# Optimization experiments

Measured on AMD Instinct MI355X. Metric: run time of the kernel, lower is better.

Reference implementation:

```python
import jax, jax.numpy as jnp
import numpy as np

PAD_IDX = 1  # matches init_kwargs pad_idx
TLEN, BATCH, D_IN = 50, 16, 512
SRC_LEN, VOCAB, CVOCAB = 200, 20000, 20400


def setup_inputs() -> dict:
    key = jax.random.key(0)
    k1, k2, k3, k4, k5, k6, k7 = jax.random.split(key, 7)
    hidden = jax.random.normal(k1, (TLEN, BATCH, D_IN), dtype=jnp.float32)
    attn = jax.random.uniform(k2, (TLEN, BATCH, SRC_LEN), dtype=jnp.float32)
    # src_map is a sparse one-hot indicator: each source position maps to one extended-vocab id
    src_ids = jax.random.randint(k3, (SRC_LEN, BATCH), 0, CVOCAB)
    src_map = jax.nn.one_hot(src_ids, CVOCAB, dtype=jnp.float32)  # (src_len, batch, cvocab)
    s = 1.0 / np.sqrt(D_IN)
    W = jax.random.uniform(k4, (VOCAB, D_IN), dtype=jnp.float32, minval=-s, maxval=s)
    b = jax.random.uniform(k5, (VOCAB,), dtype=jnp.float32, minval=-s, maxval=s)
    Wc = jax.random.uniform(k6, (1, D_IN), dtype=jnp.float32, minval=-s, maxval=s)
    bc = jax.random.uniform(k7, (1,), dtype=jnp.float32, minval=-s, maxval=s)
    return {"hidden": hidden, "attn": attn, "src_map": src_map, "W": W, "b": b, "Wc": Wc, "bc": bc}


def reference(hidden, attn, src_map, W, b, Wc, bc):
    tlen, batch, _ = hidden.shape
    src_len, _, cvocab = src_map.shape
    logits = jnp.einsum('tbd,vd->tbv', hidden, W) + b            # (tlen, batch, vocab)
    # faithful to torch: logits[:, pad_idx] = -inf (indexes the batch dim!)
    logits = logits.at[:, PAD_IDX, :].set(-jnp.inf)
    prob = jax.nn.softmax(logits, axis=1)                        # softmax over dim 1, as in source
    p_copy = jax.nn.sigmoid(jnp.einsum('tbd,od->tbo', hidden, Wc) + bc)  # (tlen, batch, 1)
    out_prob = prob * (1.0 - p_copy)                             # (tlen, batch, vocab)
    mul_attn = attn * p_copy                                     # (tlen, batch, src_len)
    # bmm over batch with one-hot src_map: effectively a scatter-add into extended vocab
    copy_prob = jnp.einsum('tbs,sbv->tbv', mul_attn, src_map)    # (tlen, batch, cvocab)
    # faithful to the split/stack/transpose permutation in the source
    flat = copy_prob.reshape(tlen * batch, cvocab)
    copy_prob = flat.reshape(batch, tlen, cvocab).swapaxes(0, 1) # (tlen, batch, cvocab)
    copy_prob = copy_prob.at[:, :, :out_prob.shape[2]].add(out_prob)
    return copy_prob
```

## Files before the change

kernel.cpp:

```cpp
#include <hip/hip_runtime.h>
#include <cstdint>
#include <cstddef>

#define TLEN    50
#define BATCH   16
#define D_IN    512
#define SRC_LEN 200
#define VOCAB   20000
#define CVOCAB  20400

typedef __bf16 bf16x8 __attribute__((ext_vector_type(8)));
typedef float  f32x4  __attribute__((ext_vector_type(4)));

#define GEMM_BLOCKS 625
#define ZERO_BLOCKS 40
#define SCAN_BLOCKS (SRC_LEN * BATCH)
#define NT 128

__global__ __launch_bounds__(256)
void pc_kernel(const float* __restrict__ hidden,
               const float* __restrict__ Wc,
               const float* __restrict__ bc,
               float* __restrict__ pc,
               __bf16* __restrict__ hbf)
{
    const int row  = blockIdx.x * 4 + (threadIdx.x >> 6);
    const int lane = threadIdx.x & 63;
    const float* h = hidden + (size_t)row * D_IN + lane * 8;
    float4 h0 = *(const float4*)(h);
    float4 h1 = *(const float4*)(h + 4);
    bf16x8 hb;
    hb[0] = (__bf16)h0.x; hb[1] = (__bf16)h0.y;
    hb[2] = (__bf16)h0.z; hb[3] = (__bf16)h0.w;
    hb[4] = (__bf16)h1.x; hb[5] = (__bf16)h1.y;
    hb[6] = (__bf16)h1.z; hb[7] = (__bf16)h1.w;
    *(bf16x8*)(hbf + (size_t)row * D_IN + lane * 8) = hb;

    float4 w0 = *(const float4*)(Wc + lane * 8);
    float4 w1 = *(const float4*)(Wc + lane * 8 + 4);
    float s = h0.x*w0.x + h0.y*w0.y + h0.z*w0.z + h0.w*w0.w
            + h1.x*w1.x + h1.y*w1.y + h1.z*w1.z + h1.w*w1.w;
    #pragma unroll
    for (int o = 1; o < 64; o <<= 1) s += __shfl_xor(s, o);
    if (lane == 0) pc[row] = 1.0f / (1.0f + __expf(-(s + bc[0])));
}

__global__ __launch_bounds__(NT)
void fused_main(const __bf16* __restrict__ hbf,
                const float* __restrict__ src_map,
                const float* __restrict__ W,
                const float* __restrict__ pc,
                float* __restrict__ out,
                int* __restrict__ src_ids)
{
    const int bid = blockIdx.x;
    const int tid = threadIdx.x;

    if (bid < GEMM_BLOCKS) {
        const int lane = tid & 63;
        const int wv   = tid >> 6;
        const int l15  = lane & 15;
        const int q    = lane >> 4;
        const int colbase = bid * 32 + wv * 16;

        bf16x8 bfrag[16];
        {
            const float* wrow = W + (size_t)(colbase + l15) * D_IN + q * 8;
            #pragma unroll
            for (int c = 0; c < 16; ++c) {
                float4 f0 = *(const float4*)(wrow + c * 32);
                float4 f1 = *(const float4*)(wrow + c * 32 + 4);
                bf16x8 bf;
                bf[0] = (__bf16)f0.x; bf[1] = (__bf16)f0.y;
                bf[2] = (__bf16)f0.z; bf[3] = (__bf16)f0.w;
                bf[4] = (__bf16)f1.x; bf[5] = (__bf16)f1.y;
                bf[6] = (__bf16)f1.z; bf[7] = (__bf16)f1.w;
                bfrag[c] = bf;
            }
            #pragma unroll
            for (int c = 0; c < 16; ++c) {
                f32x4 t = *(f32x4*)&bfrag[c];
                asm volatile("" : "+v"(t));
                bfrag[c] = *(bf16x8*)&t;
            }
        }

        for (int t = 0; t < TLEN; ++t) {
            const __bf16* arow = hbf + ((size_t)t * BATCH + l15) * D_IN + q * 8;
            f32x4 accA = {0.f, 0.f, 0.f, 0.f};
            f32x4 accB = {0.f, 0.f, 0.f, 0.f};
            #pragma unroll
            for (int c = 0; c < 16; c += 2) {
                bf16x8 a0 = *(const bf16x8*)(arow + c * 32);
                bf16x8 a1 = *(const bf16x8*)(arow + c * 32 + 32);
                accA = __builtin_amdgcn_mfma_f32_16x16x32_bf16(a0, bfrag[c],     accA, 0, 0, 0);
                accB = __builtin_amdgcn_mfma_f32_16x16x32_bf16(a1, bfrag[c + 1], accB, 0, 0, 0);
            }
            f32x4 acc = accA + accB;

            float4 pc4 = *(const float4*)(pc + t * 16 + q * 4);

            float mx = -INFINITY;
            #pragma unroll
            for (int r = 0; r < 4; ++r)
                if (q * 4 + r != 1) mx = fmaxf(mx, acc[r]);
            mx = fmaxf(mx, __shfl_xor(mx, 16));
            mx = fmaxf(mx, __shfl_xor(mx, 32));
            float e[4], s = 0.f;
            #pragma unroll
            for (int r = 0; r < 4; ++r) {
                e[r] = (q * 4 + r == 1) ? 0.f : __expf(acc[r] - mx);
                s += e[r];
            }
            s += __shfl_xor(s, 16);
            s += __shfl_xor(s, 32);
            const float inv = 1.0f / s;
            const int v = colbase + l15;
            #pragma unroll
            for (int r = 0; r < 4; ++r) {
                const int b = q * 4 + r;
                out[(size_t)(t * BATCH + b) * CVOCAB + v] = e[r] * inv * (1.0f - pc4[r]);
            }
        }
    } else if (bid < GEMM_BLOCKS + ZERO_BLOCKS) {
        const int zb = bid - GEMM_BLOCKS;
        const float4 z = {0.f, 0.f, 0.f, 0.f};
        for (int i = tid; i < 2000; i += NT) {
            const int f = zb * 2000 + i;
            const int r = f / 100;
            const int c = f % 100;
            *(float4*)(out + (size_t)r * CVOCAB + VOCAB + c * 4) = z;
        }
    } else {
        const int row = bid - GEMM_BLOCKS - ZERO_BLOCKS;
        const float4* base = (const float4*)(src_map + (size_t)row * CVOCAB);
        int found = -1;
        for (int i0 = tid; i0 < 1275; i0 += NT) {
            float4 x0 = base[i0];
            float4 x1 = base[i0 + 1275];
            float4 x2 = base[i0 + 2550];
            float4 x3 = base[i0 + 3825];
            #pragma unroll
            for (int seg = 0; seg < 4; ++seg) {
                float4 x = seg == 0 ? x0 : seg == 1 ? x1 : seg == 2 ? x2 : x3;
                const int e0 = (i0 + seg * 1275) * 4;
                if (x.x > 0.5f) found = e0;
                if (x.y > 0.5f) found = e0 + 1;
                if (x.z > 0.5f) found = e0 + 2;
                if (x.w > 0.5f) found = e0 + 3;
            }
        }
        if (found >= 0) src_ids[row] = found;
    }
}

__global__ __launch_bounds__(256)
void scatter_copy(const float* __restrict__ attn,
                  const float* __restrict__ pc,
                  const int* __restrict__ src_ids,
                  float* __restrict__ out)
{
    const int p  = blockIdx.x;
    const int si = threadIdx.x;
    if (si >= SRC_LEN) return;
    const int b  = p & 15;
    const size_t obase = (size_t)((p % TLEN) * BATCH + (p / TLEN)) * CVOCAB;
    const int id = src_ids[si * BATCH + b];
    const float val = attn[(size_t)p * SRC_LEN + si] * pc[p];
    if ((unsigned)id < (unsigned)CVOCAB)
        atomicAdd(out + obase + id, val);
}

extern "C" void kernel_launch(void* const* d_in, const int* in_sizes, int n_in,
                              void* d_out, int out_size, void* d_ws, size_t ws_size,
                              hipStream_t stream)
{
    const float* hidden  = (const float*)d_in[0];
    const float* attn    = (const float*)d_in[1];
    const float* src_map = (const float*)d_in[2];
    const float* W       = (const float*)d_in[3];
    const float* Wc      = (const float*)d_in[5];
    const float* bc      = (const float*)d_in[6];
    float* out   = (float*)d_out;

    int*    src_ids = (int*)d_ws;
    float*  pc      = (float*)((char*)d_ws + 12800);
    __bf16* hbf     = (__bf16*)((char*)d_ws + 16000);

    pc_kernel<<<dim3(200), dim3(256), 0, stream>>>(hidden, Wc, bc, pc, hbf);
    fused_main<<<dim3(GEMM_BLOCKS + ZERO_BLOCKS + SCAN_BLOCKS), dim3(NT), 0, stream>>>(
        hbf, src_map, W, pc, out, src_ids);
    scatter_copy<<<dim3(TLEN * BATCH), dim3(256), 0, stream>>>(attn, pc, src_ids, out);
}
```

Baseline: 524.0 us.

## Stage W tile in LDS and split timesteps across four waves per block

```diff
diff --git a/kernel.cpp b/kernel.cpp
--- a/kernel.cpp
+++ b/kernel.cpp
@@ -15,7 +15,7 @@
 #define GEMM_BLOCKS 625
 #define ZERO_BLOCKS 40
 #define SCAN_BLOCKS (SRC_LEN * BATCH)
-#define NT 128
+#define NT 256
 
 __global__ __launch_bounds__(256)
 void pc_kernel(const float* __restrict__ hidden,
@@ -57,69 +57,77 @@
     const int tid = threadIdx.x;
 
     if (bid < GEMM_BLOCKS) {
+        __shared__ __align__(16) __bf16 Blds[2 * 16 * 64 * 8];
+
         const int lane = tid & 63;
         const int wv   = tid >> 6;
         const int l15  = lane & 15;
         const int q    = lane >> 4;
-        const int colbase = bid * 32 + wv * 16;
-
-        bf16x8 bfrag[16];
+        const int colbase = bid * 32;
+
         {
-            const float* wrow = W + (size_t)(colbase + l15) * D_IN + q * 8;
-            #pragma unroll
-            for (int c = 0; c < 16; ++c) {
-                float4 f0 = *(const float4*)(wrow + c * 32);
-                float4 f1 = *(const float4*)(wrow + c * 32 + 4);
+            #pragma unroll
+            for (int j = 0; j < 8; ++j) {
+                const int p = wv * 8 + j;
+                const int g = p >> 4;
+                const int c = p & 15;
+                const float* src = W + (size_t)(colbase + g * 16 + l15) * D_IN
+                                     + q * 8 + c * 32;
+                float4 f0 = *(const float4*)(src);
+                float4 f1 = *(const float4*)(src + 4);
                 bf16x8 bf;
                 bf[0] = (__bf16)f0.x; bf[1] = (__bf16)f0.y;
                 bf[2] = (__bf16)f0.z; bf[3] = (__bf16)f0.w;
                 bf[4] = (__bf16)f1.x; bf[5] = (__bf16)f1.y;
                 bf[6] = (__bf16)f1.z; bf[7] = (__bf16)f1.w;
-                bfrag[c] = bf;
-            }
+                *(bf16x8*)(Blds + (size_t)(g * 16 + c) * 512 + lane * 8) = bf;
+            }
+        }
+        __syncthreads();
+
+        const int tb0 = wv * 12 + (wv < 2 ? wv : 2);
+        const int tb1 = tb0 + (wv < 2 ? 13 : 12);
+
+        for (int t = tb0; t < tb1; ++t) {
+            const __bf16* arow = hbf + ((size_t)t * BATCH + l15) * D_IN + q * 8;
+            f32x4 acc0 = {0.f, 0.f, 0.f, 0.f};
+            f32x4 acc1 = {0.f, 0.f, 0.f, 0.f};
             #pragma unroll
             for (int c = 0; c < 16; ++c) {
-                f32x4 t = *(f32x4*)&bfrag[c];
-                asm volatile("" : "+v"(t));
-                bfrag[c] = *(bf16x8*)&t;
-            }
-        }
-
-        for (int t = 0; t < TLEN; ++t) {
-            const __bf16* arow = hbf + ((size_t)t * BATCH + l15) * D_IN + q * 8;
-            f32x4 accA = {0.f, 0.f, 0.f, 0.f};
-            f32x4 accB = {0.f, 0.f, 0.f, 0.f};
-            #pragma unroll
-            for (int c = 0; c < 16; c += 2) {
-                bf16x8 a0 = *(const bf16x8*)(arow + c * 32);
-                bf16x8 a1 = *(const bf16x8*)(arow + c * 32 + 32);
-                accA = __builtin_amdgcn_mfma_f32_16x16x32_bf16(a0, bfrag[c],     accA, 0, 0, 0);
-                accB = __builtin_amdgcn_mfma_f32_16x16x32_bf16(a1, bfrag[c + 1], accB, 0, 0, 0);
-            }
-            f32x4 acc = accA + accB;
+                bf16x8 af = *(const bf16x8*)(arow + c * 32);
+                bf16x8 b0 = *(const bf16x8*)(Blds + (size_t)c * 512 + lane * 8);
+                bf16x8 b1 = *(const bf16x8*)(Blds + (size_t)(16 + c) * 512 + lane * 8);
+                acc0 = __builtin_amdgcn_mfma_f32_16x16x32_bf16(af, b0, acc0, 0, 0, 0);
+                acc1 = __builtin_amdgcn_mfma_f32_16x16x32_bf16(af, b1, acc1, 0, 0, 0);
+            }
 
             float4 pc4 = *(const float4*)(pc + t * 16 + q * 4);
 
-            float mx = -INFINITY;
-            #pragma unroll
-            for (int r = 0; r < 4; ++r)
-                if (q * 4 + r != 1) mx = fmaxf(mx, acc[r]);
-            mx = fmaxf(mx, __shfl_xor(mx, 16));
-            mx = fmaxf(mx, __shfl_xor(mx, 32));
-            float e[4], s = 0.f;
-            #pragma unroll
-            for (int r = 0; r < 4; ++r) {
-                e[r] = (q * 4 + r == 1) ? 0.f : __expf(acc[r] - mx);
-                s += e[r];
-            }
-            s += __shfl_xor(s, 16);
-            s += __shfl_xor(s, 32);
-            const float inv = 1.0f / s;
-            const int v = colbase + l15;
-            #pragma unroll
-            for (int r = 0; r < 4; ++r) {
-                const int b = q * 4 + r;
-                out[(size_t)(t * BATCH + b) * CVOCAB + v] = e[r] * inv * (1.0f - pc4[r]);
+            #pragma unroll
+            for (int g = 0; g < 2; ++g) {
+                f32x4 acc = g ? acc1 : acc0;
+                float mx = -INFINITY;
+                #pragma unroll
+                for (int r = 0; r < 4; ++r)
+                    if (q * 4 + r != 1) mx = fmaxf(mx, acc[r]);
+                mx = fmaxf(mx, __shfl_xor(mx, 16));
+                mx = fmaxf(mx, __shfl_xor(mx, 32));
+                float e[4], s = 0.f;
+                #pragma unroll
+                for (int r = 0; r < 4; ++r) {
+                    e[r] = (q * 4 + r == 1) ? 0.f : __expf(acc[r] - mx);
+                    s += e[r];
+                }
+                s += __shfl_xor(s, 16);
+                s += __shfl_xor(s, 32);
+                const float inv = 1.0f / s;
+                const int v = colbase + g * 16 + l15;
+                #pragma unroll
+                for (int r = 0; r < 4; ++r) {
+                    const int b = q * 4 + r;
+                    out[(size_t)(t * BATCH + b) * CVOCAB + v] =
+                        e[r] * inv * (1.0f - pc4[r]);
+                }
             }
         }
     } else if (bid < GEMM_BLOCKS + ZERO_BLOCKS) {
```

Measured after the change: 464.2 us. 11.4% less time.
